# Kernel tuning notes

Measured on AMD Instinct MI355X. Metric: run time of the kernel, lower is better.

## Reference

```python
import jax, jax.numpy as jnp
import numpy as np

B, S, E, H = 2, 2048, 2048, 32
D = E // H  # head_dim = 64
SCALE = D ** -0.5


def setup_inputs() -> dict:
    key = jax.random.key(0)
    ks = jax.random.split(key, 9)
    std = E ** -0.5
    return {
        "hidden_states": jax.random.normal(ks[0], (B, S, E), dtype=jnp.float32),
        "Wq": jax.random.normal(ks[1], (E, E), dtype=jnp.float32) * std,
        "bq": jax.random.normal(ks[2], (E,), dtype=jnp.float32) * 0.02,
        "Wk": jax.random.normal(ks[3], (E, E), dtype=jnp.float32) * std,
        "bk": jax.random.normal(ks[4], (E,), dtype=jnp.float32) * 0.02,
        "Wv": jax.random.normal(ks[5], (E, E), dtype=jnp.float32) * std,
        "bv": jax.random.normal(ks[6], (E,), dtype=jnp.float32) * 0.02,
        "Wo": jax.random.normal(ks[7], (E, E), dtype=jnp.float32) * std,
        "bo": jax.random.normal(ks[8], (E,), dtype=jnp.float32) * 0.02,
    }


def reference(hidden_states, Wq, bq, Wk, bk, Wv, bv, Wo, bo):
    # QKV projections (torch Linear: x @ W.T + b)
    q = hidden_states @ Wq.T + bq  # [B,S,E]
    k = hidden_states @ Wk.T + bk
    v = hidden_states @ Wv.T + bv
    # split heads -> [B,S,H,D]
    q = q.reshape(B, S, H, D)
    k = k.reshape(B, S, H, D)
    v = v.reshape(B, S, H, D)
    # causal scaled dot-product attention (prefill path of paged attention)
    scores = jnp.einsum("bqhd,bkhd->bhqk", q, k) * SCALE  # [B,H,S,S]
    causal = jnp.tril(jnp.ones((S, S), dtype=bool))
    scores = jnp.where(causal, scores, jnp.finfo(scores.dtype).min)
    probs = jax.nn.softmax(scores, axis=-1)
    attn = jnp.einsum("bhqk,bkhd->bqhd", probs, v).reshape(B, S, E)
    # output projection
    return attn @ Wo.T + bo
```

## Files before the change

### kernel.cpp

```cpp
#include <hip/hip_runtime.h>
#include <hip/hip_bf16.h>

#define B_ 2
#define S_ 2048
#define E_ 2048
#define H_ 32
#define D_ 64
#define SCALE_L2E 0.18033688f

typedef __attribute__((ext_vector_type(8))) short short8_t;
typedef __attribute__((ext_vector_type(4))) float float4_t;
typedef __attribute__((ext_vector_type(16))) float f32x16;
typedef unsigned int uint;
typedef __attribute__((ext_vector_type(4))) uint uint4_t;

__device__ __forceinline__ short f2bf(float f) {
  union { float f; unsigned u; } x; x.f = f;
  unsigned r = x.u + 0x7fffu + ((x.u >> 16) & 1u);
  return (short)(r >> 16);
}

__device__ __forceinline__ void gload_lds16(const void* g, void* l) {
  __builtin_amdgcn_global_load_lds((const __attribute__((address_space(1))) void*)g,
                                   (__attribute__((address_space(3))) void*)l, 16, 0, 0);
}

__device__ __forceinline__ uint cvt_pk_bf16(float lo, float hi) {
  uint r;
  asm volatile("v_cvt_pk_bf16_f32 %0, %1, %2" : "=v"(r) : "v"(lo), "v"(hi));
  return r;
}

__device__ __forceinline__ void pl32swap(uint& a, uint& b) {
  asm volatile("v_permlane32_swap_b32 %0, %1" : "+v"(a), "+v"(b));
}

__device__ __forceinline__ f32x16 zero16() {
  f32x16 v;
#pragma unroll
  for (int i = 0; i < 16; ++i) v[i] = 0.f;
  return v;
}

__global__ void cast_bf16_kernel(const float* __restrict__ in, short* __restrict__ out, int n4) {
  const int stride = gridDim.x * blockDim.x;
  for (int j = blockIdx.x * blockDim.x + threadIdx.x; j < n4; j += stride) {
    const float4 v = ((const float4*)in)[j];
    short4 r;
    r.x = f2bf(v.x); r.y = f2bf(v.y); r.z = f2bf(v.z); r.w = f2bf(v.w);
    ((short4*)out)[j] = r;
  }
}

__global__ void cast3_bf16(const float* __restrict__ a, const float* __restrict__ b,
                           const float* __restrict__ c, short* __restrict__ out) {
  constexpr int n4 = (E_ * E_) / 4;
  const int stride = gridDim.x * blockDim.x;
  for (int j = blockIdx.x * blockDim.x + threadIdx.x; j < 3 * n4; j += stride) {
    const float* src = (j < n4) ? a : (j < 2 * n4 ? b : c);
    const int idx = j & (n4 - 1);
    const float4 v = ((const float4*)src)[idx];
    short4 r;
    r.x = f2bf(v.x); r.y = f2bf(v.y); r.z = f2bf(v.z); r.w = f2bf(v.w);
    ((short4*)out)[j] = r;
  }
}


#define MFMA_WIN(CH)                                                                   \
  asm volatile("s_waitcnt lgkmcnt(0)" ::: "memory");                                   \
  __builtin_amdgcn_sched_barrier(0);                                                   \
  __builtin_amdgcn_s_setprio(1);                                                       \
  _Pragma("unroll")                                                                    \
  for (int i_ = 0; i_ < 8; ++i_) {                                                     \
    acc[i_][2*(CH)]   = __builtin_amdgcn_mfma_f32_16x16x32_bf16(a_[i_], b0, acc[i_][2*(CH)], 0, 0, 0);   \
    acc[i_][2*(CH)+1] = __builtin_amdgcn_mfma_f32_16x16x32_bf16(a_[i_], b1, acc[i_][2*(CH)+1], 0, 0, 0); \
  }                                                                                    \
  __builtin_amdgcn_s_setprio(0);                                                       \
  __builtin_amdgcn_s_barrier();

__global__ __launch_bounds__(512, 2) void gemm8_qkv(const short* __restrict__ A,
                                                    const short* __restrict__ Wt,
                                                    const float* __restrict__ bq,
                                                    const float* __restrict__ bk,
                                                    const float* __restrict__ bv,
                                                    short* __restrict__ Qb,
                                                    short* __restrict__ Kb,
                                                    short* __restrict__ Vb) {
  extern __shared__ __align__(16) char lds[];
  constexpr int K = E_, NT = K / 64;
  const int tid = threadIdx.x, w = tid >> 6, lane = tid & 63;
  const int wr = w >> 2, wc = w & 3;
  const int m0 = blockIdx.y * 256, n0 = blockIdx.x * 256;
  const int l15 = lane & 15, l4 = lane >> 4;

  const char* aB[2];
  const char* bB[2];
#pragma unroll
  for (int g = 0; g < 2; ++g) {
    const int r = g * 128 + w * 16 + (lane >> 2);
    const int sw = ((lane & 3) ^ ((r >> 1) & 3)) * 16;
    aB[g] = (const char*)A + (size_t)(m0 + r) * (K * 2) + sw;
    bB[g] = (const char*)Wt + (size_t)(n0 + r) * (K * 2) + sw;
  }
  const int ldsw = w * 1024;

  auto stage = [&](const char* const* base, int roff, int kt, int kh) {
    const int koff = kt * 128 + kh * 64;
#pragma unroll
    for (int g = 0; g < 2; ++g)
      gload_lds16(base[g] + koff, lds + roff + g * 8192 + ldsw);
  };

  auto ldA = [&](int dd, int ks, int i) {
    const int lr = wr * 128 + i * 16 + l15;
    return *(const short8_t*)(lds + (dd * 2 + ks) * 16384 + lr * 64 +
                              ((l4 * 16) ^ (((lr >> 1) & 3) << 4)));
  };
  auto ldB = [&](int dd, int ks, int j) {
    const int lc = wc * 64 + j * 16 + l15;
    return *(const short8_t*)(lds + 65536 + (dd * 2 + ks) * 16384 + lc * 64 +
                              ((l4 * 16) ^ (((lc >> 1) & 3) << 4)));
  };

  float4_t acc[8][4];
#pragma unroll
  for (int i = 0; i < 8; ++i)
#pragma unroll
    for (int j = 0; j < 4; ++j) acc[i][j] = (float4_t){0.f, 0.f, 0.f, 0.f};

  stage(aB, 0 * 16384, 0, 0);
  stage(bB, 65536 + 0 * 16384, 0, 0);
  stage(aB, 1 * 16384, 0, 1);
  stage(bB, 65536 + 1 * 16384, 0, 1);
  stage(aB, 2 * 16384, 1, 0);
  stage(bB, 65536 + 2 * 16384, 1, 0);
  asm volatile("s_waitcnt vmcnt(8)" ::: "memory");
  __builtin_amdgcn_s_barrier();

  short8_t a_[8], b0, b1;
  for (int t = 0; t < NT; ++t) {
    const int d = t & 1;
    asm volatile("" ::: "memory");
#pragma unroll
    for (int i = 0; i < 8; ++i) a_[i] = ldA(d, 0, i);
    b0 = ldB(d, 0, 0);
    b1 = ldB(d, 0, 1);
    if (t + 1 < NT) stage(aB, ((d ^ 1) * 2 + 1) * 16384, t + 1, 1);
    __builtin_amdgcn_s_barrier();
    MFMA_WIN(0)
    asm volatile("" ::: "memory");
    b0 = ldB(d, 0, 2);
    b1 = ldB(d, 0, 3);
    if (t + 1 < NT) stage(bB, 65536 + ((d ^ 1) * 2 + 1) * 16384, t + 1, 1);
    if (t < NT - 1) { asm volatile("s_waitcnt vmcnt(8)" ::: "memory"); }
    else           { asm volatile("s_waitcnt vmcnt(0)" ::: "memory"); }
    __builtin_amdgcn_s_barrier();
    MFMA_WIN(1)
    asm volatile("" ::: "memory");
#pragma unroll
    for (int i = 0; i < 8; ++i) a_[i] = ldA(d, 1, i);
    b0 = ldB(d, 1, 0);
    b1 = ldB(d, 1, 1);
    if (t + 2 < NT) stage(aB, (d * 2 + 0) * 16384, t + 2, 0);
    __builtin_amdgcn_s_barrier();
    MFMA_WIN(0)
    asm volatile("" ::: "memory");
    b0 = ldB(d, 1, 2);
    b1 = ldB(d, 1, 3);
    if (t + 2 < NT) stage(bB, 65536 + (d * 2 + 0) * 16384, t + 2, 0);
    if (t < NT - 1) { asm volatile("s_waitcnt vmcnt(8)" ::: "memory"); }
    else           { asm volatile("s_waitcnt vmcnt(0)" ::: "memory"); }
    __builtin_amdgcn_s_barrier();
    MFMA_WIN(1)
  }

  const int seg = n0 >> 11;
  const int ncol = n0 & 2047;
  const int rg = l4 * 4;
  if (seg == 2) {
    char* qt = lds + w * 8192;
    const int b = m0 >> 11;
    const int mloc = m0 & (S_ - 1);
#pragma unroll
    for (int sb = 0; sb < 2; ++sb) {
      asm volatile("" ::: "memory");
#pragma unroll
      for (int j = 0; j < 4; ++j) {
        const float bvv = bv[ncol + wc * 64 + j * 16 + l15];
        const int nl = j * 16 + l15;
#pragma unroll
        for (int i = 0; i < 4; ++i) {
          short4 v;
          v.x = f2bf(acc[sb * 4 + i][j][0] + bvv);
          v.y = f2bf(acc[sb * 4 + i][j][1] + bvv);
          v.z = f2bf(acc[sb * 4 + i][j][2] + bvv);
          v.w = f2bf(acc[sb * 4 + i][j][3] + bvv);
          *(short4*)(qt + nl * 128 + (((i * 16 + rg) * 2) ^ ((nl & 7) << 4))) = v;
        }
      }
      asm volatile("s_waitcnt lgkmcnt(0)" ::: "memory");
      __builtin_amdgcn_sched_barrier(0);
#pragma unroll
      for (int p = 0; p < 8; ++p) {
        const int rowd = p * 8 + (lane >> 3);
        const short8_t vv =
            *(const short8_t*)(qt + rowd * 128 + (((lane & 7) * 16) ^ ((rowd & 7) << 4)));
        *(short8_t*)(Vb + ((size_t)(b * E_ + ncol + wc * 64 + rowd)) * S_ + mloc + wr * 128 +
                     sb * 64 + (lane & 7) * 8) = vv;
      }
      asm volatile("s_waitcnt lgkmcnt(0)" ::: "memory");
      __builtin_amdgcn_sched_barrier(0);
    }
  } else {
    const float* bias = seg ? bk : bq;
    short* Out = seg ? Kb : Qb;
    const float sc = seg ? 1.0f : SCALE_L2E;
#pragma unroll
    for (int j = 0; j < 4; ++j) {
      const int col = ncol + wc * 64 + j * 16 + l15;
      const float bvv = bias[col];
#pragma unroll
      for (int i = 0; i < 8; ++i)
#pragma unroll
        for (int ii = 0; ii < 4; ++ii)
          Out[(size_t)(m0 + wr * 128 + i * 16 + rg + ii) * E_ + col] =
              f2bf((acc[i][j][ii] + bvv) * sc);
    }
  }
}

#define BM 128
#define BN 128
#define BK 32

__global__ __launch_bounds__(256) void gemm_o(const short* __restrict__ A,
                                              const short* __restrict__ Wt,
                                              const float* __restrict__ bias,
                                              float* __restrict__ Cout) {
  __shared__ __align__(16) short smem[2 * BM * BK];
  short* As = smem;
  short* Bs = smem + BM * BK;
  const int K = E_, N = E_;
  const int tid = threadIdx.x;
  const int w = tid >> 6;
  const int lane = tid & 63;
  const int m0 = blockIdx.y * BM;
  const int n0 = blockIdx.x * BN;
  const int wr = w >> 1, wc = w & 1;
  const int r16 = lane & 15;
  const int c8 = (lane >> 4) * 8;

  const int srow = lane >> 2;
  const int scol = (lane & 3) * 8;
  const short* aG0 = A  + (size_t)(m0 + (w * 2 + 0) * 16 + srow) * K + scol;
  const short* aG1 = A  + (size_t)(m0 + (w * 2 + 1) * 16 + srow) * K + scol;
  const short* bG0 = Wt + (size_t)(n0 + (w * 2 + 0) * 16 + srow) * K + scol;
  const short* bG1 = Wt + (size_t)(n0 + (w * 2 + 1) * 16 + srow) * K + scol;
  short* aL0 = As + (w * 2 + 0) * 512;
  short* aL1 = As + (w * 2 + 1) * 512;
  short* bL0 = Bs + (w * 2 + 0) * 512;
  short* bL1 = Bs + (w * 2 + 1) * 512;

  float4_t acc[4][4];
#pragma unroll
  for (int mi = 0; mi < 4; ++mi)
#pragma unroll
    for (int ni = 0; ni < 4; ++ni) acc[mi][ni] = (float4_t){0.f, 0.f, 0.f, 0.f};

  for (int kt = 0; kt < K; kt += BK) {
    __syncthreads();
    gload_lds16(aG0, aL0);
    gload_lds16(aG1, aL1);
    gload_lds16(bG0, bL0);
    gload_lds16(bG1, bL1);
    aG0 += BK; aG1 += BK; bG0 += BK; bG1 += BK;
    __syncthreads();
    short8_t af[4], bf[4];
#pragma unroll
    for (int i = 0; i < 4; ++i)
      af[i] = *(const short8_t*)(As + (wr * 64 + i * 16 + r16) * BK + c8);
#pragma unroll
    for (int i = 0; i < 4; ++i)
      bf[i] = *(const short8_t*)(Bs + (wc * 64 + i * 16 + r16) * BK + c8);
#pragma unroll
    for (int mi = 0; mi < 4; ++mi)
#pragma unroll
      for (int ni = 0; ni < 4; ++ni)
        acc[mi][ni] = __builtin_amdgcn_mfma_f32_16x16x32_bf16(af[mi], bf[ni], acc[mi][ni], 0, 0, 0);
  }

  const int rg = (lane >> 4) * 4;
  const int colbase = n0 + wc * 64;
  const int rowbase = m0 + wr * 64 + rg;
#pragma unroll
  for (int ni = 0; ni < 4; ++ni) {
    const int col = colbase + ni * 16 + r16;
    const float bvv = bias[col];
#pragma unroll
    for (int mi = 0; mi < 4; ++mi)
#pragma unroll
      for (int ii = 0; ii < 4; ++ii)
        Cout[(size_t)(rowbase + mi * 16 + ii) * N + col] = acc[mi][ni][ii] + bvv;
  }
}

__global__ __launch_bounds__(512, 2) void attn_fwd(const short* __restrict__ Qg,
                                                   const short* __restrict__ Kg,
                                                   const short* __restrict__ Vt,
                                                   short* __restrict__ Og) {
  __shared__ __align__(16) short lds[16384];
  const int tid = threadIdx.x, w = tid >> 6, lane = tid & 63;
  const int l31 = lane & 31, hh = lane >> 5;
  const int bh = blockIdx.x;
  const int b = bh >> 5, h = bh & 31;
  const int pq = blockIdx.y;

  const char* Kgb = (const char*)(Kg + (size_t)b * S_ * E_ + h * D_);
  const char* Vgb = (const char*)(Vt + (size_t)bh * 64 * S_);

  const int srow = w * 8 + (lane >> 3);
  const int sb = (lane & 7) * 16;
  const int ssw = (srow & 7) << 4;

#pragma unroll 1
  for (int ph = 0; ph < 2; ++ph) {
    const int qt = ph ? (7 - pq) : pq;
    const int q0 = qt * 256;
    const int qwmin = q0 + w * 32;
    const int qg = qwmin + l31;

    const short* qr = Qg + ((size_t)(b * S_ + qg)) * E_ + h * D_;
    short8_t qf[4];
#pragma unroll
    for (int dblk = 0; dblk < 4; ++dblk)
      qf[dblk] = *(const short8_t*)(qr + dblk * 16 + hh * 8);

    f32x16 o0 = zero16(), o1 = zero16();
    float m_run = -1e30f, l_run = 0.f;

    const int nt = 4 * qt + 4;
    const int ntw = (qwmin + 31) / 64 + 1;

    gload_lds16(Kgb + (size_t)srow * 4096 + (sb ^ ssw), lds + w * 512);
    gload_lds16(Vgb + (size_t)srow * 4096 + (sb ^ ssw), lds + 4096 + w * 512);
    __syncthreads();

    int cur = 0;
    for (int t = 0; t < nt; ++t) {
      if (t + 1 < nt) {
        const int k0n = (t + 1) * 64;
        short* kb = lds + (cur ^ 1) * 8192 + w * 512;
        gload_lds16(Kgb + (size_t)(k0n + srow) * 4096 + (sb ^ ssw), kb);
        gload_lds16(Vgb + (size_t)srow * 4096 + (size_t)k0n * 2 + (sb ^ ssw), kb + 4096);
      }

      if (t < ntw) {
        const int k0 = t * 64;
        const char* Kc = (const char*)lds + cur * 16384;
        const char* Vc = Kc + 8192;
        const int xs = (l31 & 7) << 4;

        f32x16 st0 = zero16(), st1 = zero16();
#pragma unroll
        for (int dblk = 0; dblk < 4; ++dblk) {
          const int off = (dblk * 32 + hh * 16) ^ xs;
          const short8_t kf0 = *(const short8_t*)(Kc + l31 * 128 + off);
          const short8_t kf1 = *(const short8_t*)(Kc + (32 + l31) * 128 + off);
          st0 = __builtin_amdgcn_mfma_f32_32x32x16_bf16(kf0, qf[dblk], st0, 0, 0, 0);
          st1 = __builtin_amdgcn_mfma_f32_32x32x16_bf16(kf1, qf[dblk], st1, 0, 0, 0);
        }

        if (k0 + 63 > qwmin) {
#pragma unroll
          for (int r = 0; r < 16; ++r) {
            const int kvr = k0 + ((r & 3) + 8 * (r >> 2) + 4 * hh);
            if (kvr > qg) st0[r] = -1e30f;
            if (kvr + 32 > qg) st1[r] = -1e30f;
          }
        }

        float mv = -1e30f;
#pragma unroll
        for (int r = 0; r < 16; ++r) mv = fmaxf(mv, fmaxf(st0[r], st1[r]));
        mv = fmaxf(mv, __shfl_xor(mv, 32));
        const float mnew = fmaxf(m_run, mv);
        const float alpha = exp2f(m_run - mnew);
        m_run = mnew;
        float sum = 0.f;
#pragma unroll
        for (int r = 0; r < 16; ++r) {
          st0[r] = exp2f(st0[r] - mnew);
          st1[r] = exp2f(st1[r] - mnew);
          sum += st0[r] + st1[r];
        }
        sum += __shfl_xor(sum, 32);
        l_run = l_run * alpha + sum;
        o0 = o0 * alpha;
        o1 = o1 * alpha;

        uint pk_[16];
#pragma unroll
        for (int j = 0; j < 8; ++j) pk_[j] = cvt_pk_bf16(st0[2 * j], st0[2 * j + 1]);
#pragma unroll
        for (int j = 0; j < 8; ++j) pk_[8 + j] = cvt_pk_bf16(st1[2 * j], st1[2 * j + 1]);
        pl32swap(pk_[0], pk_[2]);  pl32swap(pk_[1], pk_[3]);
        pl32swap(pk_[4], pk_[6]);  pl32swap(pk_[5], pk_[7]);
        pl32swap(pk_[8], pk_[10]); pl32swap(pk_[9], pk_[11]);
        pl32swap(pk_[12], pk_[14]); pl32swap(pk_[13], pk_[15]);
        uint4_t paw[4];
#pragma unroll
        for (int f = 0; f < 4; ++f)
          paw[f] = (uint4_t){pk_[4 * f], pk_[4 * f + 1], pk_[4 * f + 2], pk_[4 * f + 3]};

#pragma unroll
        for (int kb = 0; kb < 4; ++kb) {
          const short8_t pa = *(const short8_t*)&paw[kb];
          const int off = (kb * 32 + hh * 16) ^ xs;
          const short8_t vf0 = *(const short8_t*)(Vc + l31 * 128 + off);
          const short8_t vf1 = *(const short8_t*)(Vc + (32 + l31) * 128 + off);
          o0 = __builtin_amdgcn_mfma_f32_32x32x16_bf16(vf0, pa, o0, 0, 0, 0);
          o1 = __builtin_amdgcn_mfma_f32_32x32x16_bf16(vf1, pa, o1, 0, 0, 0);
        }
      }

      __syncthreads();
      cur ^= 1;
    }

    {
      short* ow = lds + w * 2048;
      const float inv = 1.0f / l_run;
#pragma unroll
      for (int r = 0; r < 16; ++r) {
        const int d = (r & 3) + 8 * (r >> 2) + 4 * hh;
        const int x = (l31 & 7) << 4;
        *(short*)((char*)ow + l31 * 128 + ((d * 2) ^ x)) = f2bf(o0[r] * inv);
        *(short*)((char*)ow + l31 * 128 + (((d + 32) * 2) ^ x)) = f2bf(o1[r] * inv);
      }
#pragma unroll
      for (int pz = 0; pz < 4; ++pz) {
        const int qloc = pz * 8 + (lane >> 3);
        const int sbyte = (lane & 7) * 16;
        const short8_t vv = *(const short8_t*)((char*)ow + qloc * 128 + (sbyte ^ ((qloc & 7) << 4)));
        *(short8_t*)(Og + ((size_t)(b * S_ + q0 + w * 32 + qloc)) * E_ + h * 64 + (lane & 7) * 8) = vv;
      }
    }
    __syncthreads();
  }
}

extern "C" void kernel_launch(void* const* d_in, const int* in_sizes, int n_in,
                              void* d_out, int out_size, void* d_ws, size_t ws_size,
                              hipStream_t stream) {
  const float* X  = (const float*)d_in[0];
  const float* Wq = (const float*)d_in[1];
  const float* bq = (const float*)d_in[2];
  const float* Wk = (const float*)d_in[3];
  const float* bk = (const float*)d_in[4];
  const float* Wv = (const float*)d_in[5];
  const float* bv = (const float*)d_in[6];
  const float* Wo = (const float*)d_in[7];
  const float* bo = (const float*)d_in[8];

  const size_t NX = (size_t)B_ * S_ * E_;
  const size_t NW = (size_t)E_ * E_;

  short* ws = (short*)d_ws;
  short* Xb = ws;
  short* Wb = Xb + NX;
  short* Kb = Wb + 3 * NW;
  short* Vb = Kb + NX;
  short* Qb = (short*)d_out;
  short* Ab = Xb;

  (void)hipFuncSetAttribute((const void*)gemm8_qkv,
                            hipFuncAttributeMaxDynamicSharedMemorySize, 131072);

  cast_bf16_kernel<<<2048, 256, 0, stream>>>(X, Xb, (int)(NX / 4));
  cast3_bf16<<<3072, 256, 0, stream>>>(Wq, Wk, Wv, Wb);

  gemm8_qkv<<<dim3(3 * E_ / 256, B_ * S_ / 256), 512, 131072, stream>>>(Xb, Wb, bq, bk, bv,
                                                                        Qb, Kb, Vb);

  cast_bf16_kernel<<<1024, 256, 0, stream>>>(Wo, Wb, (int)(NW / 4));

  attn_fwd<<<dim3(B_ * H_, 4), 512, 0, stream>>>(Qb, Kb, Vb, Ab);

  gemm_o<<<dim3(E_ / BN, B_ * S_ / BM), 256, 0, stream>>>(Ab, Wb, bo, (float*)d_out);
}
```

Measured before the change: 267.7 us.

## Unify QKV and output GEMMs into templated 128x256 tile kernel

```diff
diff --git a/kernel.cpp b/kernel.cpp
--- a/kernel.cpp
+++ b/kernel.cpp
@@ -66,125 +66,119 @@
   }
 }
 
-
-#define MFMA_WIN(CH)                                                                   \
-  asm volatile("s_waitcnt lgkmcnt(0)" ::: "memory");                                   \
-  __builtin_amdgcn_sched_barrier(0);                                                   \
-  __builtin_amdgcn_s_setprio(1);                                                       \
-  _Pragma("unroll")                                                                    \
-  for (int i_ = 0; i_ < 8; ++i_) {                                                     \
-    acc[i_][2*(CH)]   = __builtin_amdgcn_mfma_f32_16x16x32_bf16(a_[i_], b0, acc[i_][2*(CH)], 0, 0, 0);   \
-    acc[i_][2*(CH)+1] = __builtin_amdgcn_mfma_f32_16x16x32_bf16(a_[i_], b1, acc[i_][2*(CH)+1], 0, 0, 0); \
-  }                                                                                    \
-  __builtin_amdgcn_s_setprio(0);                                                       \
-  __builtin_amdgcn_s_barrier();
-
-__global__ __launch_bounds__(512, 2) void gemm8_qkv(const short* __restrict__ A,
-                                                    const short* __restrict__ Wt,
-                                                    const float* __restrict__ bq,
-                                                    const float* __restrict__ bk,
-                                                    const float* __restrict__ bv,
-                                                    short* __restrict__ Qb,
-                                                    short* __restrict__ Kb,
-                                                    short* __restrict__ Vb) {
+template <int MODE>
+__global__ __launch_bounds__(512, 2) void gemm8(const short* __restrict__ A,
+                                                const short* __restrict__ Wt,
+                                                const float* __restrict__ bq,
+                                                const float* __restrict__ bk,
+                                                const float* __restrict__ bv,
+                                                short* __restrict__ Qb,
+                                                short* __restrict__ Kb,
+                                                short* __restrict__ Vb,
+                                                float* __restrict__ Fout) {
   extern __shared__ __align__(16) char lds[];
   constexpr int K = E_, NT = K / 64;
   const int tid = threadIdx.x, w = tid >> 6, lane = tid & 63;
   const int wr = w >> 2, wc = w & 3;
-  const int m0 = blockIdx.y * 256, n0 = blockIdx.x * 256;
+  const int m0 = blockIdx.y * 128, n0 = blockIdx.x * 256;
   const int l15 = lane & 15, l4 = lane >> 4;
 
-  const char* aB[2];
-  const char* bB[2];
-#pragma unroll
-  for (int g = 0; g < 2; ++g) {
-    const int r = g * 128 + w * 16 + (lane >> 2);
-    const int sw = ((lane & 3) ^ ((r >> 1) & 3)) * 16;
-    aB[g] = (const char*)A + (size_t)(m0 + r) * (K * 2) + sw;
-    bB[g] = (const char*)Wt + (size_t)(n0 + r) * (K * 2) + sw;
-  }
-  const int ldsw = w * 1024;
-
-  auto stage = [&](const char* const* base, int roff, int kt, int kh) {
-    const int koff = kt * 128 + kh * 64;
-#pragma unroll
-    for (int g = 0; g < 2; ++g)
-      gload_lds16(base[g] + koff, lds + roff + g * 8192 + ldsw);
+  const int sr = lane >> 2;
+  const int ss = lane & 3;
+  const char* aBase;
+  const char* bBase0;
+  const char* bBase1;
+  {
+    const int ra = w * 16 + sr;
+    aBase = (const char*)A + (size_t)(m0 + ra) * (K * 2) + ((ss ^ ((ra >> 1) & 3)) * 16);
+    const int rb0 = 0 * 128 + w * 16 + sr;
+    bBase0 = (const char*)Wt + (size_t)(n0 + rb0) * (K * 2) + ((ss ^ ((rb0 >> 1) & 3)) * 16);
+    const int rb1 = 1 * 128 + w * 16 + sr;
+    bBase1 = (const char*)Wt + (size_t)(n0 + rb1) * (K * 2) + ((ss ^ ((rb1 >> 1) & 3)) * 16);
+  }
+
+  auto stageA = [&](int dbuf, int ks, int kt) {
+    gload_lds16(aBase + kt * 128 + ks * 64, lds + (dbuf * 2 + ks) * 8192 + w * 1024);
   };
-
-  auto ldA = [&](int dd, int ks, int i) {
-    const int lr = wr * 128 + i * 16 + l15;
-    return *(const short8_t*)(lds + (dd * 2 + ks) * 16384 + lr * 64 +
+  auto stageB = [&](int dbuf, int ks, int kt) {
+    char* base = lds + 32768 + (dbuf * 2 + ks) * 16384 + w * 1024;
+    gload_lds16(bBase0 + kt * 128 + ks * 64, base);
+    gload_lds16(bBase1 + kt * 128 + ks * 64, base + 8192);
+  };
+  auto ldA = [&](int dbuf, int ks, int i) {
+    const int lr = wr * 64 + i * 16 + l15;
+    return *(const short8_t*)(lds + (dbuf * 2 + ks) * 8192 + lr * 64 +
                               ((l4 * 16) ^ (((lr >> 1) & 3) << 4)));
   };
-  auto ldB = [&](int dd, int ks, int j) {
+  auto ldB = [&](int dbuf, int ks, int j) {
     const int lc = wc * 64 + j * 16 + l15;
-    return *(const short8_t*)(lds + 65536 + (dd * 2 + ks) * 16384 + lc * 64 +
+    return *(const short8_t*)(lds + 32768 + (dbuf * 2 + ks) * 16384 + lc * 64 +
                               ((l4 * 16) ^ (((lc >> 1) & 3) << 4)));
   };
 
-  float4_t acc[8][4];
-#pragma unroll
-  for (int i = 0; i < 8; ++i)
+  float4_t acc[4][4];
+#pragma unroll
+  for (int i = 0; i < 4; ++i)
 #pragma unroll
     for (int j = 0; j < 4; ++j) acc[i][j] = (float4_t){0.f, 0.f, 0.f, 0.f};
 
-  stage(aB, 0 * 16384, 0, 0);
-  stage(bB, 65536 + 0 * 16384, 0, 0);
-  stage(aB, 1 * 16384, 0, 1);
-  stage(bB, 65536 + 1 * 16384, 0, 1);
-  stage(aB, 2 * 16384, 1, 0);
-  stage(bB, 65536 + 2 * 16384, 1, 0);
-  asm volatile("s_waitcnt vmcnt(8)" ::: "memory");
-  __builtin_amdgcn_s_barrier();
-
-  short8_t a_[8], b0, b1;
+  stageA(0, 0, 0);
+  stageB(0, 0, 0);
+  stageA(0, 1, 0);
+  stageB(0, 1, 0);
+
+  short8_t a_[4], b_[4];
   for (int t = 0; t < NT; ++t) {
-    const int d = t & 1;
-    asm volatile("" ::: "memory");
-#pragma unroll
-    for (int i = 0; i < 8; ++i) a_[i] = ldA(d, 0, i);
-    b0 = ldB(d, 0, 0);
-    b1 = ldB(d, 0, 1);
-    if (t + 1 < NT) stage(aB, ((d ^ 1) * 2 + 1) * 16384, t + 1, 1);
-    __builtin_amdgcn_s_barrier();
-    MFMA_WIN(0)
-    asm volatile("" ::: "memory");
-    b0 = ldB(d, 0, 2);
-    b1 = ldB(d, 0, 3);
-    if (t + 1 < NT) stage(bB, 65536 + ((d ^ 1) * 2 + 1) * 16384, t + 1, 1);
-    if (t < NT - 1) { asm volatile("s_waitcnt vmcnt(8)" ::: "memory"); }
-    else           { asm volatile("s_waitcnt vmcnt(0)" ::: "memory"); }
-    __builtin_amdgcn_s_barrier();
-    MFMA_WIN(1)
-    asm volatile("" ::: "memory");
-#pragma unroll
-    for (int i = 0; i < 8; ++i) a_[i] = ldA(d, 1, i);
-    b0 = ldB(d, 1, 0);
-    b1 = ldB(d, 1, 1);
-    if (t + 2 < NT) stage(aB, (d * 2 + 0) * 16384, t + 2, 0);
-    __builtin_amdgcn_s_barrier();
-    MFMA_WIN(0)
-    asm volatile("" ::: "memory");
-    b0 = ldB(d, 1, 2);
-    b1 = ldB(d, 1, 3);
-    if (t + 2 < NT) stage(bB, 65536 + (d * 2 + 0) * 16384, t + 2, 0);
-    if (t < NT - 1) { asm volatile("s_waitcnt vmcnt(8)" ::: "memory"); }
-    else           { asm volatile("s_waitcnt vmcnt(0)" ::: "memory"); }
-    __builtin_amdgcn_s_barrier();
-    MFMA_WIN(1)
-  }
-
-  const int seg = n0 >> 11;
-  const int ncol = n0 & 2047;
+    const int c = t & 1;
+#pragma unroll
+    for (int ks = 0; ks < 2; ++ks) {
+      if (t + 1 < NT) {
+        stageA(c ^ 1, ks, t + 1);
+        stageB(c ^ 1, ks, t + 1);
+        asm volatile("s_waitcnt vmcnt(6)" ::: "memory");
+      } else if (ks == 0) {
+        asm volatile("s_waitcnt vmcnt(3)" ::: "memory");
+      } else {
+        asm volatile("s_waitcnt vmcnt(0)" ::: "memory");
+      }
+      __builtin_amdgcn_s_barrier();
+      asm volatile("" ::: "memory");
+#pragma unroll
+      for (int i = 0; i < 4; ++i) a_[i] = ldA(c, ks, i);
+#pragma unroll
+      for (int j = 0; j < 4; ++j) b_[j] = ldB(c, ks, j);
+      asm volatile("s_waitcnt lgkmcnt(0)" ::: "memory");
+      __builtin_amdgcn_sched_barrier(0);
+      __builtin_amdgcn_s_setprio(1);
+#pragma unroll
+      for (int i = 0; i < 4; ++i)
+#pragma unroll
+        for (int j = 0; j < 4; ++j)
+          acc[i][j] = __builtin_amdgcn_mfma_f32_16x16x32_bf16(a_[i], b_[j], acc[i][j], 0, 0, 0);
+      __builtin_amdgcn_s_setprio(0);
+    }
+  }
+
   const int rg = l4 * 4;
-  if (seg == 2) {
-    char* qt = lds + w * 8192;
-    const int b = m0 >> 11;
-    const int mloc = m0 & (S_ - 1);
-#pragma unroll
-    for (int sb = 0; sb < 2; ++sb) {
-      asm volatile("" ::: "memory");
+  if (MODE == 1) {
+#pragma unroll
+    for (int j = 0; j < 4; ++j) {
+      const int col = n0 + wc * 64 + j * 16 + l15;
+      const float bvv = bq[col];
+#pragma unroll
+      for (int i = 0; i < 4; ++i)
+#pragma unroll
+        for (int ii = 0; ii < 4; ++ii)
+          Fout[(size_t)(m0 + wr * 64 + i * 16 + rg + ii) * E_ + col] = acc[i][j][ii] + bvv;
+    }
+  } else {
+    const int seg = n0 >> 11;
+    const int ncol = n0 & 2047;
+    if (seg == 2) {
+      __syncthreads();
+      char* qt = lds + w * 8192;
+      const int b = m0 >> 11;
+      const int mloc = m0 & (S_ - 1);
 #pragma unroll
       for (int j = 0; j < 4; ++j) {
         const float bvv = bv[ncol + wc * 64 + j * 16 + l15];
@@ -192,10 +186,10 @@
 #pragma unroll
         for (int i = 0; i < 4; ++i) {
           short4 v;
-          v.x = f2bf(acc[sb * 4 + i][j][0] + bvv);
-          v.y = f2bf(acc[sb * 4 + i][j][1] + bvv);
-          v.z = f2bf(acc[sb * 4 + i][j][2] + bvv);
-          v.w = f2bf(acc[sb * 4 + i][j][3] + bvv);
+          v.x = f2bf(acc[i][j][0] + bvv);
+          v.y = f2bf(acc[i][j][1] + bvv);
+          v.z = f2bf(acc[i][j][2] + bvv);
+          v.w = f2bf(acc[i][j][3] + bvv);
           *(short4*)(qt + nl * 128 + (((i * 16 + rg) * 2) ^ ((nl & 7) << 4))) = v;
         }
       }
@@ -206,102 +200,25 @@
         const int rowd = p * 8 + (lane >> 3);
         const short8_t vv =
             *(const short8_t*)(qt + rowd * 128 + (((lane & 7) * 16) ^ ((rowd & 7) << 4)));
-        *(short8_t*)(Vb + ((size_t)(b * E_ + ncol + wc * 64 + rowd)) * S_ + mloc + wr * 128 +
-                     sb * 64 + (lane & 7) * 8) = vv;
-      }
-      asm volatile("s_waitcnt lgkmcnt(0)" ::: "memory");
-      __builtin_amdgcn_sched_barrier(0);
+        *(short8_t*)(Vb + ((size_t)(b * E_ + ncol + wc * 64 + rowd)) * S_ + mloc + wr * 64 +
+                     (lane & 7) * 8) = vv;
+      }
+    } else {
+      const float* bias = seg ? bk : bq;
+      short* Out = seg ? Kb : Qb;
+      const float sc = seg ? 1.0f : SCALE_L2E;
+#pragma unroll
+      for (int j = 0; j < 4; ++j) {
+        const int col = ncol + wc * 64 + j * 16 + l15;
+        const float bvv = bias[col];
+#pragma unroll
+        for (int i = 0; i < 4; ++i)
+#pragma unroll
+          for (int ii = 0; ii < 4; ++ii)
+            Out[(size_t)(m0 + wr * 64 + i * 16 + rg + ii) * E_ + col] =
+                f2bf((acc[i][j][ii] + bvv) * sc);
+      }
     }
-  } else {
-    const float* bias = seg ? bk : bq;
-    short* Out = seg ? Kb : Qb;
-    const float sc = seg ? 1.0f : SCALE_L2E;
-#pragma unroll
-    for (int j = 0; j < 4; ++j) {
-      const int col = ncol + wc * 64 + j * 16 + l15;
-      const float bvv = bias[col];
-#pragma unroll
-      for (int i = 0; i < 8; ++i)
-#pragma unroll
-        for (int ii = 0; ii < 4; ++ii)
-          Out[(size_t)(m0 + wr * 128 + i * 16 + rg + ii) * E_ + col] =
-              f2bf((acc[i][j][ii] + bvv) * sc);
-    }
-  }
-}
-
-#define BM 128
-#define BN 128
-#define BK 32
-
-__global__ __launch_bounds__(256) void gemm_o(const short* __restrict__ A,
-                                              const short* __restrict__ Wt,
-                                              const float* __restrict__ bias,
-                                              float* __restrict__ Cout) {
-  __shared__ __align__(16) short smem[2 * BM * BK];
-  short* As = smem;
-  short* Bs = smem + BM * BK;
-  const int K = E_, N = E_;
-  const int tid = threadIdx.x;
-  const int w = tid >> 6;
-  const int lane = tid & 63;
-  const int m0 = blockIdx.y * BM;
-  const int n0 = blockIdx.x * BN;
-  const int wr = w >> 1, wc = w & 1;
-  const int r16 = lane & 15;
-  const int c8 = (lane >> 4) * 8;
-
-  const int srow = lane >> 2;
-  const int scol = (lane & 3) * 8;
-  const short* aG0 = A  + (size_t)(m0 + (w * 2 + 0) * 16 + srow) * K + scol;
-  const short* aG1 = A  + (size_t)(m0 + (w * 2 + 1) * 16 + srow) * K + scol;
-  const short* bG0 = Wt + (size_t)(n0 + (w * 2 + 0) * 16 + srow) * K + scol;
-  const short* bG1 = Wt + (size_t)(n0 + (w * 2 + 1) * 16 + srow) * K + scol;
-  short* aL0 = As + (w * 2 + 0) * 512;
-  short* aL1 = As + (w * 2 + 1) * 512;
-  short* bL0 = Bs + (w * 2 + 0) * 512;
-  short* bL1 = Bs + (w * 2 + 1) * 512;
-
-  float4_t acc[4][4];
-#pragma unroll
-  for (int mi = 0; mi < 4; ++mi)
-#pragma unroll
-    for (int ni = 0; ni < 4; ++ni) acc[mi][ni] = (float4_t){0.f, 0.f, 0.f, 0.f};
-
-  for (int kt = 0; kt < K; kt += BK) {
-    __syncthreads();
-    gload_lds16(aG0, aL0);
-    gload_lds16(aG1, aL1);
-    gload_lds16(bG0, bL0);
-    gload_lds16(bG1, bL1);
-    aG0 += BK; aG1 += BK; bG0 += BK; bG1 += BK;
-    __syncthreads();
-    short8_t af[4], bf[4];
-#pragma unroll
-    for (int i = 0; i < 4; ++i)
-      af[i] = *(const short8_t*)(As + (wr * 64 + i * 16 + r16) * BK + c8);
-#pragma unroll
-    for (int i = 0; i < 4; ++i)
-      bf[i] = *(const short8_t*)(Bs + (wc * 64 + i * 16 + r16) * BK + c8);
-#pragma unroll
-    for (int mi = 0; mi < 4; ++mi)
-#pragma unroll
-      for (int ni = 0; ni < 4; ++ni)
-        acc[mi][ni] = __builtin_amdgcn_mfma_f32_16x16x32_bf16(af[mi], bf[ni], acc[mi][ni], 0, 0, 0);
-  }
-
-  const int rg = (lane >> 4) * 4;
-  const int colbase = n0 + wc * 64;
-  const int rowbase = m0 + wr * 64 + rg;
-#pragma unroll
-  for (int ni = 0; ni < 4; ++ni) {
-    const int col = colbase + ni * 16 + r16;
-    const float bvv = bias[col];
-#pragma unroll
-    for (int mi = 0; mi < 4; ++mi)
-#pragma unroll
-      for (int ii = 0; ii < 4; ++ii)
-        Cout[(size_t)(rowbase + mi * 16 + ii) * N + col] = acc[mi][ni][ii] + bvv;
   }
 }
 
@@ -474,18 +391,22 @@
   short* Qb = (short*)d_out;
   short* Ab = Xb;
 
-  (void)hipFuncSetAttribute((const void*)gemm8_qkv,
-                            hipFuncAttributeMaxDynamicSharedMemorySize, 131072);
+  (void)hipFuncSetAttribute((const void*)gemm8<0>,
+                            hipFuncAttributeMaxDynamicSharedMemorySize, 98304);
+  (void)hipFuncSetAttribute((const void*)gemm8<1>,
+                            hipFuncAttributeMaxDynamicSharedMemorySize, 98304);
 
   cast_bf16_kernel<<<2048, 256, 0, stream>>>(X, Xb, (int)(NX / 4));
   cast3_bf16<<<3072, 256, 0, stream>>>(Wq, Wk, Wv, Wb);
 
-  gemm8_qkv<<<dim3(3 * E_ / 256, B_ * S_ / 256), 512, 131072, stream>>>(Xb, Wb, bq, bk, bv,
-                                                                        Qb, Kb, Vb);
+  gemm8<0><<<dim3(3 * E_ / 256, B_ * S_ / 128), 512, 98304, stream>>>(Xb, Wb, bq, bk, bv,
+                                                                      Qb, Kb, Vb, nullptr);
 
   cast_bf16_kernel<<<1024, 256, 0, stream>>>(Wo, Wb, (int)(NW / 4));
 
   attn_fwd<<<dim3(B_ * H_, 4), 512, 0, stream>>>(Qb, Kb, Vb, Ab);
 
-  gemm_o<<<dim3(E_ / BN, B_ * S_ / BM), 256, 0, stream>>>(Ab, Wb, bo, (float*)d_out);
-}
+  gemm8<1><<<dim3(E_ / 256, B_ * S_ / 128), 512, 98304, stream>>>(Ab, Wb, bo, nullptr, nullptr,
+                                                                  nullptr, nullptr, nullptr,
+                                                                  (float*)d_out);
+}
```

Result: faster. 254.9 us (-4.8%).
